# Optimization experiments

Measured on AMD Instinct MI355X. Metric: run time of the kernel, lower is better.

## Reference

```python
import jax, jax.numpy as jnp
import numpy as np

NUM_HEAD = 32
NUM_KV_HEAD = 8
HEAD_DIM = 128
EMBED_DIM = 4096
GROUP = NUM_HEAD // NUM_KV_HEAD + 2  # 6: 4 q slots + 1 k + 1 v
TOKENS = 64


def setup_inputs() -> dict:
    key = jax.random.key(0)
    k1, k2, k3 = jax.random.split(key, 3)
    inp = jax.random.normal(k1, (TOKENS, EMBED_DIM), dtype=jnp.float32)
    # fused GQA weight layout from load_parameter: [embed_dim, num_kv_head, group, head_dim]
    weight = jax.random.normal(k2, (EMBED_DIM, NUM_KV_HEAD, GROUP, HEAD_DIM), dtype=jnp.float32) * 0.02
    bias = jax.random.normal(k3, (NUM_KV_HEAD, GROUP, HEAD_DIM), dtype=jnp.float32) * 0.02
    return {"input": inp, "weight": weight, "bias": bias}


def reference(input, weight, bias):
    # fused grouped QKV GEMM (mm_qkv_group_out):
    # out[t, kv, g, d] = sum_e input[t, e] * weight[e, kv, g, d] + bias[kv, g, d]
    out = jnp.einsum('te,ekgd->tkgd', input, weight) + bias
    T = input.shape[0]
    q = out[:, :, : GROUP - 2, :].reshape(T, NUM_HEAD * HEAD_DIM)
    k = out[:, :, GROUP - 2, :].reshape(T, NUM_KV_HEAD * HEAD_DIM)
    v = out[:, :, GROUP - 1, :].reshape(T, NUM_KV_HEAD * HEAD_DIM)
    return (q, k, v)
```

## Files before the change

### kernel.cpp

```cpp
#include <hip/hip_runtime.h>


#define N_COLS 6144
#define K_DIM  4096
#define Q_SZ   (64 * 4096)
#define K_OFF  Q_SZ
#define V_OFF  (Q_SZ + 64 * 1024)
#define OUT_ELEMS 393216
#define IN_ELEMS  262144
#define NTILES 24
#define KSPLIT 32
#define KSTEPS 4

typedef __bf16 bf16x8 __attribute__((ext_vector_type(8)));
typedef float  f32x4  __attribute__((ext_vector_type(4)));
typedef unsigned int u32x4 __attribute__((ext_vector_type(4)));

__device__ unsigned short g_abuf[IN_ELEMS];

__device__ __forceinline__ unsigned short f2bf_rne(float f) {
    unsigned int u = __float_as_uint(f);
    u += 0x7FFFu + ((u >> 16) & 1u);
    return (unsigned short)(u >> 16);
}

__device__ __forceinline__ int out_index(int t, int n) {
    const int kv = n / 768;
    const int g  = (n >> 7) % 6;
    const int d  = n & 127;
    if (g < 4)  return t * 4096 + kv * 512 + g * 128 + d;
    if (g == 4) return K_OFF + t * 1024 + kv * 128 + d;
    return V_OFF + t * 1024 + kv * 128 + d;
}

__global__ __launch_bounds__(256)
void init_kernel(const float* __restrict__ in, const float* __restrict__ bias,
                 float* __restrict__ out) {
    const int i = blockIdx.x * 256 + threadIdx.x;
    if (i < IN_ELEMS) g_abuf[i] = f2bf_rne(in[i]);
    if (i < OUT_ELEMS) {
        const int d   = i & 127;
        const int g   = (i >> 7) % 6;
        const int kvt = i / 768;
        const int kv  = kvt & 7;
        const int t   = kvt >> 3;
        out[out_index(t, kv * 768 + g * 128 + d)] = bias[(kv * 6 + g) * 128 + d];
    }
}

__device__ __forceinline__ unsigned int pack_pair(float lo, float hi) {
    return ((unsigned int)f2bf_rne(hi) << 16) | f2bf_rne(lo);
}

__global__ __launch_bounds__(256, 3)
void qkv_gemm(const float* __restrict__ w, float* __restrict__ out) {
    __shared__ u32x4 Bs[64][17];

    const int tid  = threadIdx.x;
    const int nt   = blockIdx.x % NTILES;
    const int kq   = blockIdx.x / NTILES;
    const int n0   = nt * 256;
    const int k0   = kq * (KSTEPS * 32);

    const int wid  = tid >> 6;
    const int lane = tid & 63;
    const int l15  = lane & 15;
    const int kblk = lane >> 4;

    f32x4 acc[16];
    #pragma unroll
    for (int i = 0; i < 16; ++i) acc[i] = (f32x4){0.f, 0.f, 0.f, 0.f};

    const float* wbase = w + (size_t)(k0 + 2 * wid) * N_COLS + n0 + 4 * lane;
    const unsigned short* abase = g_abuf + (wid * 16 + l15) * K_DIM + k0 + kblk * 8;

    float4 Lc[8], Ln[8];
    u32x4  Ac, An;

    #pragma unroll
    for (int r = 0; r < 4; ++r) {
        Lc[2 * r]     = *(const float4*)(wbase + (size_t)(r * 8) * N_COLS);
        Lc[2 * r + 1] = *(const float4*)(wbase + (size_t)(r * 8 + 1) * N_COLS);
    }
    Ac = *(const u32x4*)abase;

    const unsigned int* bsr = (const unsigned int*)&Bs[0][0];
    const int q = l15 >> 2, ii = l15 & 3;

    #pragma unroll
    for (int s = 0; s < KSTEPS; ++s) {
        #pragma unroll
        for (int r = 0; r < 4; ++r) {
            const float4 ra = Lc[2 * r], rb = Lc[2 * r + 1];
            u32x4 cell;
            cell[0] = pack_pair(ra.x, rb.x);
            cell[1] = pack_pair(ra.y, rb.y);
            cell[2] = pack_pair(ra.z, rb.z);
            cell[3] = pack_pair(ra.w, rb.w);
            Bs[lane][r * 4 + wid] = cell;
        }
        if (s + 1 < KSTEPS) {
            const float* wn = wbase + (size_t)((s + 1) * 32) * N_COLS;
            #pragma unroll
            for (int r = 0; r < 4; ++r) {
                Ln[2 * r]     = *(const float4*)(wn + (size_t)(r * 8) * N_COLS);
                Ln[2 * r + 1] = *(const float4*)(wn + (size_t)(r * 8 + 1) * N_COLS);
            }
            An = *(const u32x4*)(abase + (s + 1) * 32);
        }
        __syncthreads();

        const bf16x8 af = __builtin_bit_cast(bf16x8, Ac);
        #pragma unroll
        for (int nf = 0; nf < 16; ++nf) {
            const unsigned int base = (unsigned)(((nf * 4 + q) * 17 + kblk * 4) * 4 + ii);
            u32x4 bu;
            bu[0] = bsr[base];
            bu[1] = bsr[base + 4];
            bu[2] = bsr[base + 8];
            bu[3] = bsr[base + 12];
            acc[nf] = __builtin_amdgcn_mfma_f32_16x16x32_bf16(
                          af, __builtin_bit_cast(bf16x8, bu), acc[nf], 0, 0, 0);
        }
        __syncthreads();

        if (s + 1 < KSTEPS) {
            #pragma unroll
            for (int r = 0; r < 8; ++r) Lc[r] = Ln[r];
            Ac = An;
        }
    }

    #pragma unroll
    for (int nf = 0; nf < 16; ++nf) {
        const int nb = n0 + nf * 16;
        const int kv = nb / 768;
        const int g  = (nb >> 7) % 6;
        const int d  = (nb & 127) + l15;
        int base, tstride;
        if (g < 4)       { base = kv * 512 + g * 128 + d;  tstride = 4096; }
        else if (g == 4) { base = K_OFF + kv * 128 + d;    tstride = 1024; }
        else             { base = V_OFF + kv * 128 + d;    tstride = 1024; }
        const int t0 = wid * 16 + kblk * 4;
        #pragma unroll
        for (int r = 0; r < 4; ++r)
            atomicAdd(&out[base + (t0 + r) * tstride], acc[nf][r]);
    }
}

extern "C" void kernel_launch(void* const* d_in, const int* in_sizes, int n_in,
                              void* d_out, int out_size, void* d_ws, size_t ws_size,
                              hipStream_t stream) {
    const float* in   = (const float*)d_in[0];
    const float* w    = (const float*)d_in[1];
    const float* bias = (const float*)d_in[2];
    float* out = (float*)d_out;

    init_kernel<<<(OUT_ELEMS + 255) / 256, 256, 0, stream>>>(in, bias, out);
    qkv_gemm<<<NTILES * KSPLIT, 256, 0, stream>>>(w, out);
}
```

Baseline: 182.7 us.

## Replace atomic split-K with partial buffers, async LDS weight loads, and reduce kernel

```diff
diff --git a/kernel.cpp b/kernel.cpp
--- a/kernel.cpp
+++ b/kernel.cpp
@@ -7,21 +7,23 @@
 #define K_OFF  Q_SZ
 #define V_OFF  (Q_SZ + 64 * 1024)
 #define OUT_ELEMS 393216
-#define IN_ELEMS  262144
-#define NTILES 24
-#define KSPLIT 32
-#define KSTEPS 4
+#define NT     48
+#define KSPLIT 16
+#define BK     32
+#define TILES  8
 
 typedef __bf16 bf16x8 __attribute__((ext_vector_type(8)));
 typedef float  f32x4  __attribute__((ext_vector_type(4)));
 typedef unsigned int u32x4 __attribute__((ext_vector_type(4)));
 
-__device__ unsigned short g_abuf[IN_ELEMS];
-
 __device__ __forceinline__ unsigned short f2bf_rne(float f) {
     unsigned int u = __float_as_uint(f);
     u += 0x7FFFu + ((u >> 16) & 1u);
     return (unsigned short)(u >> 16);
+}
+
+__device__ __forceinline__ unsigned int pack_pair(float lo, float hi) {
+    return ((unsigned int)f2bf_rne(hi) << 16) | f2bf_rne(lo);
 }
 
 __device__ __forceinline__ int out_index(int t, int n) {
@@ -33,119 +35,109 @@
     return V_OFF + t * 1024 + kv * 128 + d;
 }
 
-__global__ __launch_bounds__(256)
-void init_kernel(const float* __restrict__ in, const float* __restrict__ bias,
-                 float* __restrict__ out) {
-    const int i = blockIdx.x * 256 + threadIdx.x;
-    if (i < IN_ELEMS) g_abuf[i] = f2bf_rne(in[i]);
-    if (i < OUT_ELEMS) {
-        const int d   = i & 127;
-        const int g   = (i >> 7) % 6;
-        const int kvt = i / 768;
-        const int kv  = kvt & 7;
-        const int t   = kvt >> 3;
-        out[out_index(t, kv * 768 + g * 128 + d)] = bias[(kv * 6 + g) * 128 + d];
-    }
-}
+#define GLDS(gp, lp) __builtin_amdgcn_global_load_lds(                        \
+    (const __attribute__((address_space(1))) void*)(gp),                      \
+    (__attribute__((address_space(3))) void*)(lp), 16, 0, 0)
 
-__device__ __forceinline__ unsigned int pack_pair(float lo, float hi) {
-    return ((unsigned int)f2bf_rne(hi) << 16) | f2bf_rne(lo);
-}
-
-__global__ __launch_bounds__(256, 3)
-void qkv_gemm(const float* __restrict__ w, float* __restrict__ out) {
-    __shared__ u32x4 Bs[64][17];
+__global__ __launch_bounds__(256, 4)
+void qkv_gemm(const float* __restrict__ in, const float* __restrict__ w,
+              float* __restrict__ part) {
+    __shared__ float Ws[BK * 128];
 
     const int tid  = threadIdx.x;
-    const int nt   = blockIdx.x % NTILES;
-    const int kq   = blockIdx.x / NTILES;
-    const int n0   = nt * 256;
-    const int k0   = kq * (KSTEPS * 32);
-
+    const int nt   = blockIdx.x % NT;
+    const int kq   = blockIdx.x / NT;
+    const int n0   = nt * 128;
+    const int k0   = kq * 256;
     const int wid  = tid >> 6;
     const int lane = tid & 63;
     const int l15  = lane & 15;
     const int kblk = lane >> 4;
 
-    f32x4 acc[16];
+    f32x4 acc[2][4];
     #pragma unroll
-    for (int i = 0; i < 16; ++i) acc[i] = (f32x4){0.f, 0.f, 0.f, 0.f};
+    for (int a = 0; a < 2; ++a)
+        #pragma unroll
+        for (int b = 0; b < 4; ++b) acc[a][b] = (f32x4){0.f, 0.f, 0.f, 0.f};
 
-    const float* wbase = w + (size_t)(k0 + 2 * wid) * N_COLS + n0 + 4 * lane;
-    const unsigned short* abase = g_abuf + (wid * 16 + l15) * K_DIM + k0 + kblk * 8;
+    #pragma unroll 1
+    for (int s = 0; s < TILES; ++s) {
+        const int kc = k0 + s * BK;
 
-    float4 Lc[8], Ln[8];
-    u32x4  Ac, An;
-
-    #pragma unroll
-    for (int r = 0; r < 4; ++r) {
-        Lc[2 * r]     = *(const float4*)(wbase + (size_t)(r * 8) * N_COLS);
-        Lc[2 * r + 1] = *(const float4*)(wbase + (size_t)(r * 8 + 1) * N_COLS);
-    }
-    Ac = *(const u32x4*)abase;
-
-    const unsigned int* bsr = (const unsigned int*)&Bs[0][0];
-    const int q = l15 >> 2, ii = l15 & 3;
-
-    #pragma unroll
-    for (int s = 0; s < KSTEPS; ++s) {
+        const float* wr = w + (size_t)kc * N_COLS + n0;
         #pragma unroll
         for (int r = 0; r < 4; ++r) {
-            const float4 ra = Lc[2 * r], rb = Lc[2 * r + 1];
-            u32x4 cell;
-            cell[0] = pack_pair(ra.x, rb.x);
-            cell[1] = pack_pair(ra.y, rb.y);
-            cell[2] = pack_pair(ra.z, rb.z);
-            cell[3] = pack_pair(ra.w, rb.w);
-            Bs[lane][r * 4 + wid] = cell;
+            const int u = r * 256 + tid;
+            GLDS(wr + (size_t)(u >> 5) * N_COLS + (u & 31) * 4, &Ws[u * 4]);
         }
-        if (s + 1 < KSTEPS) {
-            const float* wn = wbase + (size_t)((s + 1) * 32) * N_COLS;
+
+        float4 alo[4], ahi[4];
+        #pragma unroll
+        for (int mi = 0; mi < 4; ++mi) {
+            const float* ap = in + (size_t)(mi * 16 + l15) * K_DIM + kc + kblk * 8;
+            alo[mi] = *(const float4*)ap;
+            ahi[mi] = *(const float4*)(ap + 4);
+        }
+
+        __syncthreads();
+
+        u32x4 af[4];
+        #pragma unroll
+        for (int mi = 0; mi < 4; ++mi) {
+            af[mi][0] = pack_pair(alo[mi].x, alo[mi].y);
+            af[mi][1] = pack_pair(alo[mi].z, alo[mi].w);
+            af[mi][2] = pack_pair(ahi[mi].x, ahi[mi].y);
+            af[mi][3] = pack_pair(ahi[mi].z, ahi[mi].w);
+        }
+
+        #pragma unroll
+        for (int nfi = 0; nfi < 2; ++nfi) {
+            const int nb = (wid * 2 + nfi) * 16 + l15;
+            float bf[8];
+            #pragma unroll
+            for (int j = 0; j < 8; ++j)
+                bf[j] = Ws[(kblk * 8 + j) * 128 + nb];
+            u32x4 bu;
+            #pragma unroll
+            for (int j2 = 0; j2 < 4; ++j2)
+                bu[j2] = pack_pair(bf[2 * j2], bf[2 * j2 + 1]);
+
+            const bf16x8 bv = __builtin_bit_cast(bf16x8, bu);
+            #pragma unroll
+            for (int mi = 0; mi < 4; ++mi)
+                acc[nfi][mi] = __builtin_amdgcn_mfma_f32_16x16x32_bf16(
+                    __builtin_bit_cast(bf16x8, af[mi]), bv, acc[nfi][mi], 0, 0, 0);
+        }
+
+        __syncthreads();
+    }
+
+    float* pb = part + (size_t)kq * OUT_ELEMS;
+    #pragma unroll
+    for (int nfi = 0; nfi < 2; ++nfi) {
+        const int n = n0 + (wid * 2 + nfi) * 16 + l15;
+        #pragma unroll
+        for (int mi = 0; mi < 4; ++mi) {
             #pragma unroll
             for (int r = 0; r < 4; ++r) {
-                Ln[2 * r]     = *(const float4*)(wn + (size_t)(r * 8) * N_COLS);
-                Ln[2 * r + 1] = *(const float4*)(wn + (size_t)(r * 8 + 1) * N_COLS);
+                const int t = mi * 16 + kblk * 4 + r;
+                pb[(size_t)t * N_COLS + n] = acc[nfi][mi][r];
             }
-            An = *(const u32x4*)(abase + (s + 1) * 32);
-        }
-        __syncthreads();
-
-        const bf16x8 af = __builtin_bit_cast(bf16x8, Ac);
-        #pragma unroll
-        for (int nf = 0; nf < 16; ++nf) {
-            const unsigned int base = (unsigned)(((nf * 4 + q) * 17 + kblk * 4) * 4 + ii);
-            u32x4 bu;
-            bu[0] = bsr[base];
-            bu[1] = bsr[base + 4];
-            bu[2] = bsr[base + 8];
-            bu[3] = bsr[base + 12];
-            acc[nf] = __builtin_amdgcn_mfma_f32_16x16x32_bf16(
-                          af, __builtin_bit_cast(bf16x8, bu), acc[nf], 0, 0, 0);
-        }
-        __syncthreads();
-
-        if (s + 1 < KSTEPS) {
-            #pragma unroll
-            for (int r = 0; r < 8; ++r) Lc[r] = Ln[r];
-            Ac = An;
         }
     }
+}
 
+__global__ __launch_bounds__(256)
+void qkv_reduce(const float* __restrict__ part, const float* __restrict__ bias,
+                float* __restrict__ out) {
+    const int i = blockIdx.x * 256 + threadIdx.x;
+    const int t = i / N_COLS;
+    const int n = i % N_COLS;
+    float s = bias[n];
     #pragma unroll
-    for (int nf = 0; nf < 16; ++nf) {
-        const int nb = n0 + nf * 16;
-        const int kv = nb / 768;
-        const int g  = (nb >> 7) % 6;
-        const int d  = (nb & 127) + l15;
-        int base, tstride;
-        if (g < 4)       { base = kv * 512 + g * 128 + d;  tstride = 4096; }
-        else if (g == 4) { base = K_OFF + kv * 128 + d;    tstride = 1024; }
-        else             { base = V_OFF + kv * 128 + d;    tstride = 1024; }
-        const int t0 = wid * 16 + kblk * 4;
-        #pragma unroll
-        for (int r = 0; r < 4; ++r)
-            atomicAdd(&out[base + (t0 + r) * tstride], acc[nf][r]);
-    }
+    for (int kq = 0; kq < KSPLIT; ++kq)
+        s += part[(size_t)kq * OUT_ELEMS + i];
+    out[out_index(t, n)] = s;
 }
 
 extern "C" void kernel_launch(void* const* d_in, const int* in_sizes, int n_in,
@@ -154,8 +146,9 @@
     const float* in   = (const float*)d_in[0];
     const float* w    = (const float*)d_in[1];
     const float* bias = (const float*)d_in[2];
-    float* out = (float*)d_out;
+    float* out  = (float*)d_out;
+    float* part = (float*)d_ws;
 
-    init_kernel<<<(OUT_ELEMS + 255) / 256, 256, 0, stream>>>(in, bias, out);
-    qkv_gemm<<<NTILES * KSPLIT, 256, 0, stream>>>(w, out);
+    qkv_gemm<<<NT * KSPLIT, 256, 0, stream>>>(in, w, part);
+    qkv_reduce<<<OUT_ELEMS / 256, 256, 0, stream>>>(part, bias, out);
 }
```

After: 163.9 us. 1.12x faster.
